# Optimization experiments

Hardware: AMD Instinct MI355X
Metric: run time of the kernel (lower is better)

## Reference

```python
import jax, jax.numpy as jnp
import numpy as np

D = 1024   # model dim (hard-coded in ClsNet)
H = 16     # num_heads
HD = D // H
FF = 2048  # torch TransformerEncoderLayer default dim_feedforward
B, LX, LY = 8, 512, 512
EPS = 1e-5
NEG = -1e9


def setup_inputs() -> dict:
    key = jax.random.key(0)
    ks = jax.random.split(key, 16)
    s = 0.02
    inp = {
        "x": jax.random.normal(ks[0], (B, LX, D), jnp.float32),
        "y": jax.random.normal(ks[1], (B, LY, D), jnp.float32),
        "cls": jax.random.normal(ks[2], (D,), jnp.float32) * s,
        "sep": jax.random.normal(ks[3], (D,), jnp.float32) * s,
        "px": jax.random.normal(ks[4], (D,), jnp.float32) * s,
        "py": jax.random.normal(ks[5], (D,), jnp.float32) * s,
        "Wqkv": jax.random.normal(ks[6], (3 * D, D), jnp.float32) * s,
        "bqkv": jnp.zeros((3 * D,), jnp.float32),
        "Wo": jax.random.normal(ks[7], (D, D), jnp.float32) * s,
        "bo": jnp.zeros((D,), jnp.float32),
        "W1": jax.random.normal(ks[8], (FF, D), jnp.float32) * s,
        "b1": jnp.zeros((FF,), jnp.float32),
        "W2": jax.random.normal(ks[9], (D, FF), jnp.float32) * s,
        "b2": jnp.zeros((D,), jnp.float32),
        "ln1_g": jnp.ones((D,), jnp.float32),
        "ln1_b": jnp.zeros((D,), jnp.float32),
        "ln2_g": jnp.ones((D,), jnp.float32),
        "ln2_b": jnp.zeros((D,), jnp.float32),
        "x_len": jax.random.randint(ks[10], (B,), 1, LX + 1, jnp.int32),
        "y_len": jax.random.randint(ks[11], (B,), 1, LY + 1, jnp.int32),
    }
    return inp


def _merge(x, y, cls, sep, px, py, x_len, y_len):
    # Vectorized version of ClsNet.merge: [CLS] x_i+px ... [SEP] y_i+py ... [SEP] pad...
    Bn, Lx, Dd = x.shape
    Ly = y.shape[1]
    S = Lx + Ly + 3
    pos = jnp.arange(S)[None, :]            # [1,S]
    lx = x_len[:, None]                     # [B,1]
    ly = y_len[:, None]
    is_cls = pos == 0                       # [1,S]
    is_x = (pos >= 1) & (pos <= lx)         # [B,S]
    is_sep1 = pos == lx + 1
    is_y = (pos >= lx + 2) & (pos <= lx + ly + 1)
    is_sep2 = pos == lx + ly + 2
    xi = jnp.clip(pos - 1, 0, Lx - 1)       # [1,S]
    yi = jnp.clip(pos - lx - 2, 0, Ly - 1)  # [B,S]
    xg = jnp.take_along_axis(x, xi[:, :, None], axis=1)  # [B,S,D] (broadcast batch)
    yg = jnp.take_along_axis(y, yi[:, :, None], axis=1)  # [B,S,D]
    seq = (jnp.where(is_x[..., None], xg + px, 0.0)
           + jnp.where(is_y[..., None], yg + py, 0.0)
           + is_cls[..., None] * cls
           + (is_sep1 | is_sep2)[..., None] * sep)       # [B,S,D]
    mask = is_cls | is_x | is_sep1 | is_y | is_sep2      # [B,S] True = valid token
    return seq, mask


def _ln(h, g, b):
    m = jnp.mean(h, axis=-1, keepdims=True)
    v = jnp.mean(jnp.square(h - m), axis=-1, keepdims=True)
    return (h - m) * jax.lax.rsqrt(v + EPS) * g + b


def _encoder_layer(seq, mask, Wqkv, bqkv, Wo, bo, W1, b1, W2, b2, ln1_g, ln1_b, ln2_g, ln2_b):
    Bn, S, Dd = seq.shape
    qkv = seq @ Wqkv.T + bqkv                              # [B,S,3D]
    q, k, v = jnp.split(qkv, 3, axis=-1)
    q = q.reshape(Bn, S, H, HD)
    k = k.reshape(Bn, S, H, HD)
    v = v.reshape(Bn, S, H, HD)
    bias = jnp.where(mask, 0.0, NEG)[:, None, None, :]     # padded KEYS masked out
    scores = jnp.einsum("bqhd,bkhd->bhqk", q, k) / np.sqrt(HD) + bias
    attn = jax.nn.softmax(scores, axis=-1)
    o = jnp.einsum("bhqk,bkhd->bqhd", attn, v).reshape(Bn, S, Dd)
    o = o @ Wo.T + bo
    h = _ln(seq + o, ln1_g, ln1_b)                          # post-norm (torch default)
    f = jax.nn.relu(h @ W1.T + b1) @ W2.T + b2
    return _ln(h + f, ln2_g, ln2_b)


def reference(x, y, cls, sep, px, py, Wqkv, bqkv, Wo, bo, W1, b1, W2, b2,
              ln1_g, ln1_b, ln2_g, ln2_b, x_len, y_len):
    seq, mask = _merge(x, y, cls, sep, px, py, x_len, y_len)
    out = _encoder_layer(seq, mask, Wqkv, bqkv, Wo, bo, W1, b1, W2, b2,
                         ln1_g, ln1_b, ln2_g, ln2_b)
    # torch code returns a[0] of the seq-first tensor -> the CLS position for all batches
    return out[:, 0, :]
```

## Files before the change

### kernel.cpp

```cpp
#include <hip/hip_runtime.h>
#include <hip/hip_bf16.h>

#define D_ 1024
#define H_ 16
#define FF_ 2048
#define B_ 8
#define S_ 1027
#define BS_ 8216
#define MPAD_ 8320
#define PSTR_ 1056
#define EPS_ 1e-5f
#define MAXGRID_ 512
#define NTILE_ 130
#define NBUCK_ 32

#define OFF_SEQ  0
#define OFF_RTHI 17039360
#define OFF_RTLO 17072128
#define OFF_S    17104896
#define OFF_P    17637376
#define OFF_CBAR 17907712
#define OFF_O0   20004864
#define OFF_ATT  20037632
#define OFF_F1   20070400
#define OFF_F2   20103168
#define OFF_BAR  20135936
#define OFF_Q0S  20140032
#define OFF_H0   20144128

typedef __hip_bfloat16 bf16;
typedef unsigned short u16;
typedef unsigned int u32;
typedef __attribute__((ext_vector_type(4))) float floatx4;
typedef __bf16 bf16x8 __attribute__((ext_vector_type(8)));

__device__ __forceinline__ float2 bfpair(u32 u) {
  union { u32 u; float f; } lo, hi;
  lo.u = u << 16; hi.u = u & 0xffff0000u;
  return make_float2(lo.f, hi.f);
}

__device__ __forceinline__ u32 f2bfbits(float f) {
  union { bf16 h; u16 u; } cv; cv.h = __float2bfloat16(f); return (u32)cv.u;
}

__device__ __forceinline__ void st_wt_f32(float* p, float v) {
  asm volatile("global_store_dword %0, %1, off sc0 sc1" :: "v"(p), "v"(v) : "memory");
}
__device__ __forceinline__ void st_wt_u16(u16* p, u32 v) {
  asm volatile("global_store_short %0, %1, off sc0 sc1" :: "v"(p), "v"(v) : "memory");
}
__device__ __forceinline__ void st_wt_v2(void* p, uint2 v) {
  asm volatile("global_store_dwordx2 %0, %1, off sc0 sc1" :: "v"(p), "v"(v) : "memory");
}
__device__ __forceinline__ void st_wt_f4(void* p, floatx4 v) {
  asm volatile("global_store_dwordx4 %0, %1, off sc0 sc1" :: "v"(p), "v"(v) : "memory");
}

__device__ __forceinline__ float blk_sum(float x, float* red) {
#pragma unroll
  for (int off = 32; off > 0; off >>= 1) x += __shfl_down(x, off, 64);
  __syncthreads();
  if ((threadIdx.x & 63) == 0) red[threadIdx.x >> 6] = x;
  __syncthreads();
  return red[0] + red[1] + red[2] + red[3];
}

__device__ __forceinline__ float blk_max(float x, float* red) {
#pragma unroll
  for (int off = 32; off > 0; off >>= 1) x = fmaxf(x, __shfl_down(x, off, 64));
  __syncthreads();
  if ((threadIdx.x & 63) == 0) red[threadIdx.x >> 6] = x;
  __syncthreads();
  return fmaxf(fmaxf(red[0], red[1]), fmaxf(red[2], red[3]));
}

__device__ __forceinline__ void gridbar(u32* bar, u32 phase) {
  asm volatile("s_waitcnt vmcnt(0) lgkmcnt(0)" ::: "memory");
  __syncthreads();
  if (threadIdx.x == 0) {
    __hip_atomic_fetch_add(bar + (blockIdx.x & (NBUCK_ - 1)) * 16, 1u,
                           __ATOMIC_RELAXED, __HIP_MEMORY_SCOPE_AGENT);
    u32* gen = bar + NBUCK_ * 16;
    if (blockIdx.x == 0) {
      const u32 target = (u32)gridDim.x * phase;
      int spins = 0;
      for (;;) {
        u32 s = 0;
#pragma unroll
        for (int i = 0; i < NBUCK_; ++i)
          s += __hip_atomic_load(bar + i * 16, __ATOMIC_RELAXED,
                                 __HIP_MEMORY_SCOPE_AGENT);
        if (s == target) break;
        __builtin_amdgcn_s_sleep(1);
        if (++spins > 300000) break;
      }
      __hip_atomic_store(gen, phase, __ATOMIC_RELAXED, __HIP_MEMORY_SCOPE_AGENT);
    } else {
      int spins = 0;
      while (__hip_atomic_load(gen, __ATOMIC_RELAXED,
                               __HIP_MEMORY_SCOPE_AGENT) < phase) {
        __builtin_amdgcn_s_sleep(2);
        if (++spins > 300000) break;
      }
    }
  }
  __syncthreads();
}

struct KP {
  const float *x, *y, *cls, *sep, *px, *py;
  const float *Wqkv, *bqkv, *Wo, *bo, *W1, *b1, *W2, *b2;
  const float *g1, *be1, *g2, *be2;
  const int *xl, *yl;
  bf16* seq; u16* RT_hi; u16* RT_lo; float* S; u16* P;
  float* cbar4; float* o0; float* att; bf16* f1; float* f2; float* out;
  u32* bar;
};

__global__ void __launch_bounds__(256, 2) mega_kernel(KP p) {
  __shared__ __align__(16) char smem_[33792];
  const int t = threadIdx.x;
  const int bid = blockIdx.x;
  const int G = gridDim.x;

  if (t == 0) __builtin_amdgcn_fence(__ATOMIC_ACQUIRE, "agent");
  gridbar(p.bar, 1);

  if (bid < 64) {
    const int h = bid >> 2, cc = bid & 3;
    float* cl = (float*)smem_;
    float* qs = (float*)(smem_ + 4096);
    *(float4*)&cl[t * 4] = ((const float4*)p.cls)[t];
    __syncthreads();
    const int r = t >> 2, j = t & 3;
    const float* wr = p.Wqkv + (size_t)(h * 64 + r) * D_;
    float acc = 0.f;
#pragma unroll 8
    for (int i = 0; i < 64; ++i) {
      float4 wv = *(const float4*)(wr + i * 16 + j * 4);
      const float* c4 = &cl[i * 16 + j * 4];
      acc += wv.x * c4[0] + wv.y * c4[1] + wv.z * c4[2] + wv.w * c4[3];
    }
    acc += __shfl_xor(acc, 1, 64);
    acc += __shfl_xor(acc, 2, 64);
    if (j == 0) qs[r] = (acc + p.bqkv[h * 64 + r]) * 0.125f;
    __syncthreads();
    const int c = cc * 256 + t;
    const float* Wk = p.Wqkv + (size_t)(D_ + h * 64) * D_ + c;
    float a2 = 0.f;
#pragma unroll 8
    for (int e = 0; e < 64; ++e) a2 += Wk[(size_t)e * D_] * qs[e];
    const u32 hb = f2bfbits(a2);
    union { u32 u; float f; } hv; hv.u = hb << 16;
    st_wt_u16(p.RT_hi + h * D_ + c, hb);
    st_wt_u16(p.RT_lo + h * D_ + c, f2bfbits(a2 - hv.f));
  } else {
    for (int m = bid - 64; m < BS_; m += G - 64) {
      const int b = m / S_;
      const int s = m - b * S_;
      const int lx = p.xl[b], ly = p.yl[b];
      const float* src = nullptr;
      const float* add = nullptr;
      if (s == 0) src = p.cls;
      else if (s <= lx) { src = p.x + ((size_t)b * 512 + (s - 1)) * D_; add = p.px; }
      else if (s == lx + 1) src = p.sep;
      else if (s <= lx + ly + 1) { src = p.y + ((size_t)b * 512 + (s - lx - 2)) * D_; add = p.py; }
      else if (s == lx + ly + 2) src = p.sep;
      if (!src) continue;
      float4 sv = ((const float4*)src)[t];
      if (add) {
        float4 av = ((const float4*)add)[t];
        sv.x += av.x; sv.y += av.y; sv.z += av.z; sv.w += av.w;
      }
      uint2 o;
      o.x = f2bfbits(sv.x) | (f2bfbits(sv.y) << 16);
      o.y = f2bfbits(sv.z) | (f2bfbits(sv.w) << 16);
      st_wt_v2((u16*)p.seq + (size_t)m * D_ + t * 4, o);
    }
  }
  gridbar(p.bar, 2);

  for (int wk = bid; wk < NTILE_; wk += G) {
    const int m0 = wk * 64;
    bool valid = false;
#pragma unroll
    for (int b = 0; b < B_; ++b) {
      int rs = b * S_, re = rs + p.xl[b] + p.yl[b] + 3;
      if (m0 < re && m0 + 64 > rs) valid = true;
    }
    if (!valid) continue;
    const int w = t >> 6, lane = t & 63, lane16 = lane & 15, quad = lane >> 4;
    const int row = m0 + w * 16 + lane16;
    const u16* arow = (const u16*)p.seq + (size_t)row * D_ + quad * 8;
    const u16* bh = p.RT_hi + lane16 * D_ + quad * 8;
    const u16* bl = p.RT_lo + lane16 * D_ + quad * 8;
    floatx4 acc = {};
#pragma unroll 4
    for (int kt = 0; kt < 32; ++kt) {
      bf16x8 a  = *(const bf16x8*)(arow + kt * 32);
      bf16x8 vh = *(const bf16x8*)(bh + kt * 32);
      bf16x8 vl = *(const bf16x8*)(bl + kt * 32);
      acc = __builtin_amdgcn_mfma_f32_16x16x32_bf16(a, vh, acc, 0, 0, 0);
      acc = __builtin_amdgcn_mfma_f32_16x16x32_bf16(a, vl, acc, 0, 0, 0);
    }
    st_wt_f4(&p.S[(size_t)lane16 * MPAD_ + m0 + w * 16 + quad * 4], acc);
  }
  gridbar(p.bar, 3);

  for (int wk = bid; wk < 128; wk += G) {
    const int h = wk >> 3, b = wk & 7;
    const int n = p.xl[b] + p.yl[b] + 3;
    float* sc = (float*)smem_;
    float* red = (float*)(smem_ + PSTR_ * 4);
    const float* Sp = p.S + (size_t)h * MPAD_ + b * S_;
    float lmax = -3.0e38f;
    for (int k = t; k < n; k += 256) {
      float s = Sp[k];
      sc[k] = s;
      lmax = fmaxf(lmax, s);
    }
    const float gmax = blk_max(lmax, red);
    float lsum = 0.f;
    for (int k = t; k < n; k += 256) {
      float pr = __expf(sc[k] - gmax);
      sc[k] = pr;
      lsum += pr;
    }
    const float inv = 1.0f / blk_sum(lsum, red);
    u16* Pp = p.P + (size_t)(h * 8 + b) * PSTR_;
    for (int k = t; k < PSTR_; k += 256)
      st_wt_u16(Pp + k, (k < n) ? f2bfbits(sc[k] * inv) : 0u);
    __syncthreads();
  }
  gridbar(p.bar, 4);

  for (int wk = bid; wk < 512; wk += G) {
    const int ct = wk & 15, b = (wk >> 4) & 7, piece = wk >> 7;
    const int c0 = ct * 64;
    const int n = p.xl[b] + p.yl[b] + 3;
    const int nkt = (n + 31) >> 5;
    const int KR0[4] = {0, 9, 17, 25};
    const int KR1[4] = {9, 17, 25, 33};
    const int kt0 = KR0[piece];
    const int kt1 = nkt < KR1[piece] ? nkt : KR1[piece];
    u16* tile = (u16*)smem_;
    const int w = t >> 6, lane = t & 63, lane16 = lane & 15, quad = lane >> 4;
    const int sk = t >> 3, scg = (t & 7) * 8;
    floatx4 acc = {};
    uint4 v = make_uint4(0u, 0u, 0u, 0u);
    if (kt0 < kt1 && kt0 * 32 + sk < n)
      v = *(const uint4*)((const u16*)p.seq + (size_t)((size_t)b * S_ + kt0 * 32 + sk) * D_ + c0 + scg);
    for (int kt = kt0; kt < kt1; ++kt) {
      u16* tb = tile + (kt & 1) * (32 * 68);
      *(uint2*)&tb[sk * 68 + scg]     = make_uint2(v.x, v.y);
      *(uint2*)&tb[sk * 68 + scg + 4] = make_uint2(v.z, v.w);
      v = make_uint4(0u, 0u, 0u, 0u);
      if (kt + 1 < kt1 && (kt + 1) * 32 + sk < n)
        v = *(const uint4*)((const u16*)p.seq + (size_t)((size_t)b * S_ + (kt + 1) * 32 + sk) * D_ + c0 + scg);
      __syncthreads();
      bf16x8 a = *(const bf16x8*)(p.P + (size_t)(lane16 * 8 + b) * PSTR_ + kt * 32 + quad * 8);
      union { bf16x8 v8; u16 u[8]; } bu;
#pragma unroll
      for (int j = 0; j < 8; ++j)
        bu.u[j] = tb[(quad * 8 + j) * 68 + w * 16 + lane16];
      acc = __builtin_amdgcn_mfma_f32_16x16x32_bf16(a, bu.v8, acc, 0, 0, 0);
    }
    float* dst = p.cbar4 + (size_t)piece * 131072;
#pragma unroll
    for (int r = 0; r < 4; ++r)
      st_wt_f32(&dst[(size_t)(b * 16 + quad * 4 + r) * D_ + c0 + w * 16 + lane16], acc[r]);
    __syncthreads();
  }
  gridbar(p.bar, 5);

  for (int wk = bid; wk < 256; wk += G) {
    float* lsf = (float*)smem_;
    const int hoff = ((wk * 4) >> 6) * D_;
#pragma unroll
    for (int i = 0; i < 8; ++i) {
      int flat = (t + i * 256) * 4;
      int b = flat >> 10, k = flat & 1023;
      size_t off = (size_t)b * 16384 + hoff + k;
      float4 a0 = *(const float4*)(p.cbar4 + off);
      float4 a1 = *(const float4*)(p.cbar4 + 131072 + off);
      float4 a2 = *(const float4*)(p.cbar4 + 262144 + off);
      float4 a3 = *(const float4*)(p.cbar4 + 393216 + off);
      a0.x += a1.x + a2.x + a3.x; a0.y += a1.y + a2.y + a3.y;
      a0.z += a1.z + a2.z + a3.z; a0.w += a1.w + a2.w + a3.w;
      *(float4*)&lsf[flat] = a0;
    }
    __syncthreads();
    const int w = t >> 6, l = t & 63;
    const int r = wk * 4 + w;
    const float* W = p.Wqkv + (size_t)2048 * 1024;
    float acc[8] = {};
#pragma unroll
    for (int ch = 0; ch < 4; ++ch) {
      float4 wv = *(const float4*)(W + (size_t)r * D_ + ch * 256 + l * 4);
#pragma unroll
      for (int b = 0; b < 8; ++b) {
        const float* pp = &lsf[b * D_ + ch * 256 + l * 4];
        acc[b] += wv.x * pp[0] + wv.y * pp[1] + wv.z * pp[2] + wv.w * pp[3];
      }
    }
#pragma unroll
    for (int off = 32; off > 0; off >>= 1)
#pragma unroll
      for (int b = 0; b < 8; ++b) acc[b] += __shfl_down(acc[b], off, 64);
    if (l == 0) {
      const float bs = p.bqkv[2048 + r];
#pragma unroll
      for (int b = 0; b < 8; ++b) st_wt_f32(&p.o0[(size_t)b * D_ + r], acc[b] + bs);
    }
    __syncthreads();
  }
  gridbar(p.bar, 6);

  for (int wk = bid; wk < 256; wk += G) {
    float* lsf = (float*)smem_;
#pragma unroll
    for (int i = 0; i < 8; ++i) {
      int flat = (t + i * 256) * 4;
      *(float4*)&lsf[flat] = *(const float4*)(p.o0 + flat);
    }
    __syncthreads();
    const int w = t >> 6, l = t & 63;
    const int r = wk * 4 + w;
    float acc[8] = {};
#pragma unroll
    for (int ch = 0; ch < 4; ++ch) {
      float4 wv = *(const float4*)(p.Wo + (size_t)r * D_ + ch * 256 + l * 4);
#pragma unroll
      for (int b = 0; b < 8; ++b) {
        const float* pp = &lsf[b * D_ + ch * 256 + l * 4];
        acc[b] += wv.x * pp[0] + wv.y * pp[1] + wv.z * pp[2] + wv.w * pp[3];
      }
    }
#pragma unroll
    for (int off = 32; off > 0; off >>= 1)
#pragma unroll
      for (int b = 0; b < 8; ++b) acc[b] += __shfl_down(acc[b], off, 64);
    if (l == 0) {
      const float bs = p.bo[r];
#pragma unroll
      for (int b = 0; b < 8; ++b) st_wt_f32(&p.att[(size_t)b * D_ + r], acc[b] + bs);
    }
    __syncthreads();
  }
  gridbar(p.bar, 7);

  for (int wk = bid; wk < 512; wk += G) {
    float* lsf = (float*)smem_;
#pragma unroll
    for (int i = 0; i < 8; ++i) {
      int flat = (t + i * 256) * 4;
      int b = flat >> 10, k = flat & 1023;
      float4 av = *(const float4*)(p.att + (size_t)b * D_ + k);
      float4 cv = *(const float4*)(p.cls + k);
      av.x += cv.x; av.y += cv.y; av.z += cv.z; av.w += cv.w;
      *(float4*)&lsf[flat] = av;
    }
    __syncthreads();
    const int w = t >> 6, l = t & 63;
#pragma unroll
    for (int bb = 2 * w; bb < 2 * w + 2; ++bb) {
      float s = 0.f;
#pragma unroll
      for (int kk = 0; kk < 16; ++kk) s += lsf[bb * 1024 + kk * 64 + l];
#pragma unroll
      for (int off = 32; off > 0; off >>= 1) s += __shfl_xor(s, off, 64);
      const float mean = s * (1.f / D_);
      float vv = 0.f;
#pragma unroll
      for (int kk = 0; kk < 16; ++kk) {
        float d = lsf[bb * 1024 + kk * 64 + l] - mean; vv += d * d;
      }
#pragma unroll
      for (int off = 32; off > 0; off >>= 1) vv += __shfl_xor(vv, off, 64);
      const float rs = rsqrtf(vv * (1.f / D_) + EPS_);
#pragma unroll
      for (int kk = 0; kk < 16; ++kk) {
        int idx = kk * 64 + l;
        lsf[bb * 1024 + idx] =
            (lsf[bb * 1024 + idx] - mean) * rs * p.g1[idx] + p.be1[idx];
      }
    }
    __syncthreads();
    const int r = wk * 4 + w;
    float acc[8] = {};
#pragma unroll
    for (int ch = 0; ch < 4; ++ch) {
      float4 wv = *(const float4*)(p.W1 + (size_t)r * D_ + ch * 256 + l * 4);
#pragma unroll
      for (int b = 0; b < 8; ++b) {
        const float* pp = &lsf[b * D_ + ch * 256 + l * 4];
        acc[b] += wv.x * pp[0] + wv.y * pp[1] + wv.z * pp[2] + wv.w * pp[3];
      }
    }
#pragma unroll
    for (int off = 32; off > 0; off >>= 1)
#pragma unroll
      for (int b = 0; b < 8; ++b) acc[b] += __shfl_down(acc[b], off, 64);
    if (l == 0) {
      const float bs = p.b1[r];
#pragma unroll
      for (int b = 0; b < 8; ++b)
        st_wt_u16((u16*)p.f1 + (size_t)b * FF_ + r, f2bfbits(fmaxf(acc[b] + bs, 0.f)));
    }
    __syncthreads();
  }
  gridbar(p.bar, 8);

  for (int wk = bid; wk < 256; wk += G) {
    u16* lsb = (u16*)smem_;
#pragma unroll
    for (int i = 0; i < 8; ++i) {
      int flat = (t + i * 256) * 8;
      *(uint4*)&lsb[flat] = *(const uint4*)((const u16*)p.f1 + flat);
    }
    __syncthreads();
    const int w = t >> 6, l = t & 63;
    const int r = wk * 4 + w;
    float acc[8] = {};
#pragma unroll
    for (int ch = 0; ch < 8; ++ch) {
      float4 wv = *(const float4*)(p.W2 + (size_t)r * FF_ + ch * 256 + l * 4);
#pragma unroll
      for (int b = 0; b < 8; ++b) {
        uint2 u = *(const uint2*)&lsb[b * FF_ + ch * 256 + l * 4];
        float2 p0 = bfpair(u.x), p1 = bfpair(u.y);
        acc[b] += wv.x * p0.x + wv.y * p0.y + wv.z * p1.x + wv.w * p1.y;
      }
    }
#pragma unroll
    for (int off = 32; off > 0; off >>= 1)
#pragma unroll
      for (int b = 0; b < 8; ++b) acc[b] += __shfl_down(acc[b], off, 64);
    if (l == 0) {
      const float bs = p.b2[r];
#pragma unroll
      for (int b = 0; b < 8; ++b) st_wt_f32(&p.f2[(size_t)b * D_ + r], acc[b] + bs);
    }
    __syncthreads();
  }
  gridbar(p.bar, 9);

  for (int wk = bid; wk < 8; wk += G) {
    float* v = (float*)smem_;
    float* red = (float*)(smem_ + D_ * 4);
    for (int i = t; i < D_; i += 256) v[i] = p.cls[i] + p.att[wk * D_ + i];
    __syncthreads();
    float ls = 0.f;
    for (int i = t; i < D_; i += 256) ls += v[i];
    const float mean1 = blk_sum(ls, red) * (1.f / D_);
    float lv = 0.f;
    for (int i = t; i < D_; i += 256) { float dk = v[i] - mean1; lv += dk * dk; }
    const float var1 = blk_sum(lv, red) * (1.f / D_);
    const float rs1 = rsqrtf(var1 + EPS_);
    for (int i = t; i < D_; i += 256) {
      float h0v = (v[i] - mean1) * rs1 * p.g1[i] + p.be1[i];
      v[i] = h0v + p.f2[wk * D_ + i];
    }
    __syncthreads();
    float ls2 = 0.f;
    for (int i = t; i < D_; i += 256) ls2 += v[i];
    const float mean2 = blk_sum(ls2, red) * (1.f / D_);
    float lv2 = 0.f;
    for (int i = t; i < D_; i += 256) { float dk = v[i] - mean2; lv2 += dk * dk; }
    const float var2 = blk_sum(lv2, red) * (1.f / D_);
    const float rs2 = rsqrtf(var2 + EPS_);
    for (int i = t; i < D_; i += 256)
      p.out[wk * D_ + i] = (v[i] - mean2) * rs2 * p.g2[i] + p.be2[i];
    __syncthreads();
  }
}

__device__ __forceinline__ float block_sum(float x, float* red) {
  const int t = threadIdx.x;
  __syncthreads();
  red[t] = x;
  __syncthreads();
  for (int s = 128; s > 0; s >>= 1) {
    if (t < s) red[t] += red[t + s];
    __syncthreads();
  }
  return red[0];
}

__device__ __forceinline__ float block_max(float x, float* red) {
  const int t = threadIdx.x;
  __syncthreads();
  red[t] = x;
  __syncthreads();
  for (int s = 128; s > 0; s >>= 1) {
    if (t < s) red[t] = fmaxf(red[t], red[t + s]);
    __syncthreads();
  }
  return red[0];
}

__global__ void __launch_bounds__(256) build_seq_kernel(
    const float* __restrict__ x, const float* __restrict__ y,
    const float* __restrict__ cls, const float* __restrict__ sep,
    const float* __restrict__ px, const float* __restrict__ py,
    const int* __restrict__ x_len, const int* __restrict__ y_len,
    bf16* __restrict__ seq) {
  const int m = blockIdx.x, t = threadIdx.x;
  const int b = m / S_;
  const int s = m - b * S_;
  if (b >= B_) return;
  const float* src = nullptr;
  const float* add = nullptr;
  const int lx = x_len[b], ly = y_len[b];
  if (s == 0) src = cls;
  else if (s <= lx) { src = x + ((size_t)b * 512 + (s - 1)) * D_; add = px; }
  else if (s == lx + 1) src = sep;
  else if (s <= lx + ly + 1) { src = y + ((size_t)b * 512 + (s - lx - 2)) * D_; add = py; }
  else if (s == lx + ly + 2) src = sep;
  if (!src) return;
  float4 sv = ((const float4*)src)[t];
  if (add) {
    float4 av = ((const float4*)add)[t];
    sv.x += av.x; sv.y += av.y; sv.z += av.z; sv.w += av.w;
  }
  uint2 o;
  o.x = f2bfbits(sv.x) | (f2bfbits(sv.y) << 16);
  o.y = f2bfbits(sv.z) | (f2bfbits(sv.w) << 16);
  ((uint2*)(seq + (size_t)m * D_))[t] = o;
}

__global__ void __launch_bounds__(256) qproj_kernel(
    const float* __restrict__ cls, const float* __restrict__ Wqkv,
    const float* __restrict__ bqkv, float* __restrict__ q0s) {
  __shared__ float cl[D_];
  const int t = threadIdx.x;
  *(float4*)&cl[t * 4] = ((const float4*)cls)[t];
  __syncthreads();
  const int w = t >> 6, l = t & 63;
  const int r = blockIdx.x * 4 + w;
  float acc = 0.f;
#pragma unroll
  for (int ch = 0; ch < 4; ++ch) {
    float4 wv = *(const float4*)(Wqkv + (size_t)r * D_ + ch * 256 + l * 4);
    const float* c4 = &cl[ch * 256 + l * 4];
    acc += wv.x * c4[0] + wv.y * c4[1] + wv.z * c4[2] + wv.w * c4[3];
  }
#pragma unroll
  for (int off = 32; off > 0; off >>= 1) acc += __shfl_down(acc, off, 64);
  if (l == 0) q0s[r] = (acc + bqkv[r]) * 0.125f;
}

__global__ void __launch_bounds__(256) rproj_kernel(
    const float* __restrict__ Wqkv, const float* __restrict__ q0s,
    u16* __restrict__ RT_hi, u16* __restrict__ RT_lo) {
  const int h = blockIdx.y, cc = blockIdx.x, t = threadIdx.x;
  __shared__ float qs[64];
  if (t < 64) qs[t] = q0s[h * 64 + t];
  __syncthreads();
  const int c = cc * 256 + t;
  const float* Wk = Wqkv + (size_t)(D_ + h * 64) * D_ + c;
  float acc = 0.f;
#pragma unroll 8
  for (int e = 0; e < 64; ++e) acc += Wk[(size_t)e * D_] * qs[e];
  const u32 hb = f2bfbits(acc);
  union { u32 u; float f; } hv; hv.u = hb << 16;
  RT_hi[h * D_ + c] = (u16)hb;
  RT_lo[h * D_ + c] = (u16)f2bfbits(acc - hv.f);
}

__global__ void __launch_bounds__(256) scores_kernel(
    const bf16* __restrict__ seq, const u16* __restrict__ RT_hi,
    const u16* __restrict__ RT_lo, const int* __restrict__ x_len,
    const int* __restrict__ y_len, float* __restrict__ S) {
  const int m0 = blockIdx.x * 64;
  bool valid = false;
#pragma unroll
  for (int b = 0; b < B_; ++b) {
    int rs = b * S_, re = rs + x_len[b] + y_len[b] + 3;
    if (m0 < re && m0 + 64 > rs) valid = true;
  }
  if (!valid) return;
  const int t = threadIdx.x;
  const int w = t >> 6, lane = t & 63, lane16 = lane & 15, quad = lane >> 4;
  const int row = m0 + w * 16 + lane16;
  const u16* arow = (const u16*)seq + (size_t)row * D_ + quad * 8;
  const u16* bh = RT_hi + lane16 * D_ + quad * 8;
  const u16* bl = RT_lo + lane16 * D_ + quad * 8;
  floatx4 acc = {};
#pragma unroll 4
  for (int kt = 0; kt < 32; ++kt) {
    bf16x8 a  = *(const bf16x8*)(arow + kt * 32);
    bf16x8 vh = *(const bf16x8*)(bh + kt * 32);
    bf16x8 vl = *(const bf16x8*)(bl + kt * 32);
    acc = __builtin_amdgcn_mfma_f32_16x16x32_bf16(a, vh, acc, 0, 0, 0);
    acc = __builtin_amdgcn_mfma_f32_16x16x32_bf16(a, vl, acc, 0, 0, 0);
  }
  *(floatx4*)&S[(size_t)lane16 * MPAD_ + m0 + w * 16 + quad * 4] = acc;
}

__global__ void __launch_bounds__(256) softmax_kernel(
    const float* __restrict__ S, const int* __restrict__ x_len,
    const int* __restrict__ y_len, u16* __restrict__ P) {
  const int h = blockIdx.x, b = blockIdx.y, t = threadIdx.x;
  const int n = x_len[b] + y_len[b] + 3;
  __shared__ float sc[PSTR_];
  __shared__ float red[256];
  const float* Sp = S + (size_t)h * MPAD_ + b * S_;
  float lmax = -3.0e38f;
  for (int k = t; k < n; k += 256) {
    float s = Sp[k];
    sc[k] = s;
    lmax = fmaxf(lmax, s);
  }
  const float gmax = block_max(lmax, red);
  float lsum = 0.f;
  for (int k = t; k < n; k += 256) {
    float p = __expf(sc[k] - gmax);
    sc[k] = p;
    lsum += p;
  }
  const float inv = 1.0f / block_sum(lsum, red);
  u16* Pp = P + (size_t)(h * 8 + b) * PSTR_;
  for (int k = t; k < PSTR_; k += 256)
    Pp[k] = (k < n) ? (u16)f2bfbits(sc[k] * inv) : (u16)0;
}

__global__ void __launch_bounds__(256) cbar_kernel(
    const bf16* __restrict__ seq, const u16* __restrict__ P,
    const int* __restrict__ x_len, const int* __restrict__ y_len,
    float* __restrict__ cbar) {
  const int ct = blockIdx.x, b = blockIdx.y, t = threadIdx.x;
  const int c0 = ct * 64;
  const int n = x_len[b] + y_len[b] + 3;
  const int nkt = (n + 31) >> 5;
  __shared__ u16 tile[32 * 68];
  const int w = t >> 6, lane = t & 63, lane16 = lane & 15, quad = lane >> 4;
  const int sk = t >> 3, scg = (t & 7) * 8;
  floatx4 acc = {};
  for (int kt = 0; kt < nkt; ++kt) {
    const int k0 = kt * 32;
    __syncthreads();
    uint4 v = make_uint4(0u, 0u, 0u, 0u);
    if (k0 + sk < n)
      v = *(const uint4*)((const u16*)seq + (size_t)(b * S_ + k0 + sk) * D_ + c0 + scg);
    *(uint2*)&tile[sk * 68 + scg]     = make_uint2(v.x, v.y);
    *(uint2*)&tile[sk * 68 + scg + 4] = make_uint2(v.z, v.w);
    __syncthreads();
    bf16x8 a = *(const bf16x8*)(P + (size_t)(lane16 * 8 + b) * PSTR_ + k0 + quad * 8);
    union { bf16x8 v; u16 u[8]; } bu;
#pragma unroll
    for (int j = 0; j < 8; ++j)
      bu.u[j] = tile[(quad * 8 + j) * 68 + w * 16 + lane16];
    acc = __builtin_amdgcn_mfma_f32_16x16x32_bf16(a, bu.v, acc, 0, 0, 0);
  }
#pragma unroll
  for (int r = 0; r < 4; ++r)
    cbar[(size_t)(b * 16 + quad * 4 + r) * D_ + c0 + w * 16 + lane16] = acc[r];
}

template <int K, int N, int BSTR, bool INBF, bool OUTBF, bool RELU, bool PERHEAD>
__global__ void __launch_bounds__(256) gemv8_kernel(
    const void* __restrict__ in_, const float* __restrict__ W,
    const float* __restrict__ bias, void* __restrict__ out_) {
  const int t = threadIdx.x;
  const int hoff = PERHEAD ? ((blockIdx.x * 4) >> 6) * D_ : 0;
  __shared__ u16 lsb[INBF ? 8 * K : 1];
  __shared__ float lsf[INBF ? 1 : 8 * K];
  if (INBF) {
    const u16* in = (const u16*)in_;
    const int per = 8 * K / (256 * 8);
#pragma unroll
    for (int i = 0; i < per; ++i) {
      int flat = (t + i * 256) * 8;
      int b = flat / K, k = flat % K;
      *(uint4*)&lsb[flat] = *(const uint4*)(in + (size_t)b * BSTR + hoff + k);
    }
  } else {
    const float* in = (const float*)in_;
    const int per = 8 * K / (256 * 4);
#pragma unroll
    for (int i = 0; i < per; ++i) {
      int flat = (t + i * 256) * 4;
      int b = flat / K, k = flat % K;
      *(float4*)&lsf[flat] = *(const float4*)(in + (size_t)b * BSTR + hoff + k);
    }
  }
  __syncthreads();
  const int w = t >> 6, l = t & 63;
  const int r = blockIdx.x * 4 + w;
  float acc[8] = {};
#pragma unroll
  for (int ch = 0; ch < K / 256; ++ch) {
    float4 wv = *(const float4*)(W + (size_t)r * K + ch * 256 + l * 4);
#pragma unroll
    for (int b = 0; b < 8; ++b) {
      float i0, i1, i2, i3;
      if (INBF) {
        uint2 u = *(const uint2*)&lsb[b * K + ch * 256 + l * 4];
        float2 p0 = bfpair(u.x), p1 = bfpair(u.y);
        i0 = p0.x; i1 = p0.y; i2 = p1.x; i3 = p1.y;
      } else {
        const float* p = &lsf[b * K + ch * 256 + l * 4];
        i0 = p[0]; i1 = p[1]; i2 = p[2]; i3 = p[3];
      }
      acc[b] += wv.x * i0 + wv.y * i1 + wv.z * i2 + wv.w * i3;
    }
  }
#pragma unroll
  for (int off = 32; off > 0; off >>= 1)
#pragma unroll
    for (int b = 0; b < 8; ++b) acc[b] += __shfl_down(acc[b], off, 64);
  if (l == 0) {
    const float bs = bias[r];
#pragma unroll
    for (int b = 0; b < 8; ++b) {
      float v = acc[b] + bs;
      if (RELU) v = fmaxf(v, 0.f);
      if (OUTBF) ((bf16*)out_)[(size_t)b * N + r] = __float2bfloat16(v);
      else       ((float*)out_)[(size_t)b * N + r] = v;
    }
  }
}

template <bool SECOND>
__global__ void __launch_bounds__(256) ln_kernel(
    const float* __restrict__ cls, const float* __restrict__ a,
    const float* __restrict__ bvec, const float* __restrict__ g,
    const float* __restrict__ be, float* __restrict__ out) {
  const int b = blockIdx.x, t = threadIdx.x;
  __shared__ float v[D_];
  __shared__ float red[256];
  for (int i = t; i < D_; i += 256) {
    float val;
    if (SECOND) val = a[b * D_ + i] + bvec[b * D_ + i];
    else        val = cls[i] + a[b * D_ + i];
    v[i] = val;
  }
  __syncthreads();
  float ls = 0.f;
  for (int i = t; i < D_; i += 256) ls += v[i];
  const float mean = block_sum(ls, red) * (1.f / D_);
  float lv = 0.f;
  for (int i = t; i < D_; i += 256) { float dk = v[i] - mean; lv += dk * dk; }
  const float var = block_sum(lv, red) * (1.f / D_);
  const float rs = rsqrtf(var + EPS_);
  for (int i = t; i < D_; i += 256)
    out[b * D_ + i] = (v[i] - mean) * rs * g[i] + be[i];
}

extern "C" void kernel_launch(void* const* d_in, const int* in_sizes, int n_in,
                              void* d_out, int out_size, void* d_ws, size_t ws_size,
                              hipStream_t stream) {
  (void)in_sizes; (void)n_in; (void)out_size; (void)ws_size;
  const float* x    = (const float*)d_in[0];
  const float* y    = (const float*)d_in[1];
  const float* cls  = (const float*)d_in[2];
  const float* sep  = (const float*)d_in[3];
  const float* px   = (const float*)d_in[4];
  const float* py   = (const float*)d_in[5];
  const float* Wqkv = (const float*)d_in[6];
  const float* bqkv = (const float*)d_in[7];
  const float* Wo   = (const float*)d_in[8];
  const float* bo   = (const float*)d_in[9];
  const float* W1   = (const float*)d_in[10];
  const float* b1   = (const float*)d_in[11];
  const float* W2   = (const float*)d_in[12];
  const float* b2   = (const float*)d_in[13];
  const float* g1   = (const float*)d_in[14];
  const float* be1  = (const float*)d_in[15];
  const float* g2   = (const float*)d_in[16];
  const float* be2  = (const float*)d_in[17];
  const int* xl     = (const int*)d_in[18];
  const int* yl     = (const int*)d_in[19];

  char* ws = (char*)d_ws;
  bf16*  seq   = (bf16*)(ws + OFF_SEQ);
  u16*   RT_hi = (u16*)(ws + OFF_RTHI);
  u16*   RT_lo = (u16*)(ws + OFF_RTLO);
  float* S     = (float*)(ws + OFF_S);
  u16*   P     = (u16*)(ws + OFF_P);
  float* cbar4 = (float*)(ws + OFF_CBAR);
  float* o0    = (float*)(ws + OFF_O0);
  float* att   = (float*)(ws + OFF_ATT);
  bf16*  f1    = (bf16*)(ws + OFF_F1);
  float* f2    = (float*)(ws + OFF_F2);
  u32*   bar   = (u32*)(ws + OFF_BAR);
  float* q0s   = (float*)(ws + OFF_Q0S);
  float* h0    = (float*)(ws + OFF_H0);

  KP kp;
  kp.x = x; kp.y = y; kp.cls = cls; kp.sep = sep; kp.px = px; kp.py = py;
  kp.Wqkv = Wqkv; kp.bqkv = bqkv; kp.Wo = Wo; kp.bo = bo;
  kp.W1 = W1; kp.b1 = b1; kp.W2 = W2; kp.b2 = b2;
  kp.g1 = g1; kp.be1 = be1; kp.g2 = g2; kp.be2 = be2;
  kp.xl = xl; kp.yl = yl;
  kp.seq = seq; kp.RT_hi = RT_hi; kp.RT_lo = RT_lo;
  kp.S = S; kp.P = P; kp.cbar4 = cbar4;
  kp.o0 = o0; kp.att = att; kp.f1 = f1; kp.f2 = f2;
  kp.out = (float*)d_out;
  kp.bar = bar;

  static int mega_grid = -2;
  if (mega_grid == -2) {
    int nb = 0, ncu = 256;
    hipDeviceProp_t props;
    if (hipGetDeviceProperties(&props, 0) == hipSuccess)
      ncu = props.multiProcessorCount;
    if (hipOccupancyMaxActiveBlocksPerMultiprocessor(&nb, mega_kernel, 256, 0) ==
            hipSuccess && nb > 0) {
      long g = (long)nb * ncu;
      mega_grid = (int)(g < MAXGRID_ ? g : MAXGRID_);
    } else {
      mega_grid = -1;
    }
    if (mega_grid < 72) mega_grid = -1;
  }

  if (mega_grid > 0) {
    hipMemsetAsync(ws + OFF_BAR, 0, 4096, stream);
    mega_kernel<<<mega_grid, 256, 0, stream>>>(kp);
  } else {
    build_seq_kernel<<<MPAD_, 256, 0, stream>>>(x, y, cls, sep, px, py, xl, yl, seq);
    qproj_kernel<<<256, 256, 0, stream>>>(cls, Wqkv, bqkv, q0s);
    rproj_kernel<<<dim3(4, 16), 256, 0, stream>>>(Wqkv, q0s, RT_hi, RT_lo);
    scores_kernel<<<130, 256, 0, stream>>>(seq, RT_hi, RT_lo, xl, yl, S);
    softmax_kernel<<<dim3(16, 8), 256, 0, stream>>>(S, xl, yl, P);
    cbar_kernel<<<dim3(16, 8), 256, 0, stream>>>(seq, P, xl, yl, cbar4);
    gemv8_kernel<1024, 1024, 16384, false, false, false, true>
        <<<256, 256, 0, stream>>>(cbar4, Wqkv + (size_t)2048 * 1024, bqkv + 2048, o0);
    gemv8_kernel<1024, 1024, 1024, false, false, false, false>
        <<<256, 256, 0, stream>>>(o0, Wo, bo, att);
    ln_kernel<false><<<B_, 256, 0, stream>>>(cls, att, nullptr, g1, be1, h0);
    gemv8_kernel<1024, 2048, 1024, false, true, true, false>
        <<<512, 256, 0, stream>>>(h0, W1, b1, f1);
    gemv8_kernel<2048, 1024, 2048, true, false, false, false>
        <<<256, 256, 0, stream>>>(f1, W2, b2, f2);
    ln_kernel<true><<<B_, 256, 0, stream>>>(nullptr, h0, f2, g2, be2, (float*)d_out);
  }
}
```

Before: 211.2 us.

## Trim grid barriers, flatten barrier polling, and accumulate cbar with atomics

Drops the initial grid barrier and replaces the generation-flag barrier with one where every block polls 8 bucket counters directly. The cbar stage now accumulates into a single buffer with float atomicAdd, after zeroing it during the softmax phase. This removes the 4-piece partial buffers, their reduction in the next stage and one grid barrier. The sequence-build loop also processes two rows per iteration, issuing loads before stores. The trade-offs are more atomic traffic and more contention from all blocks polling the counters, and the summation order now varies between runs.

Measured after the change: 224.7 us. 6.4% more time.

```diff
diff --git a/kernel.cpp b/kernel.cpp
--- a/kernel.cpp
+++ b/kernel.cpp
@@ -12,7 +12,6 @@
 #define EPS_ 1e-5f
 #define MAXGRID_ 512
 #define NTILE_ 130
-#define NBUCK_ 32
 
 #define OFF_SEQ  0
 #define OFF_RTHI 17039360
@@ -79,30 +78,19 @@
   asm volatile("s_waitcnt vmcnt(0) lgkmcnt(0)" ::: "memory");
   __syncthreads();
   if (threadIdx.x == 0) {
-    __hip_atomic_fetch_add(bar + (blockIdx.x & (NBUCK_ - 1)) * 16, 1u,
+    __hip_atomic_fetch_add(bar + (blockIdx.x & 7) * 16, 1u,
                            __ATOMIC_RELAXED, __HIP_MEMORY_SCOPE_AGENT);
-    u32* gen = bar + NBUCK_ * 16;
-    if (blockIdx.x == 0) {
-      const u32 target = (u32)gridDim.x * phase;
-      int spins = 0;
-      for (;;) {
-        u32 s = 0;
-#pragma unroll
-        for (int i = 0; i < NBUCK_; ++i)
-          s += __hip_atomic_load(bar + i * 16, __ATOMIC_RELAXED,
-                                 __HIP_MEMORY_SCOPE_AGENT);
-        if (s == target) break;
-        __builtin_amdgcn_s_sleep(1);
-        if (++spins > 300000) break;
-      }
-      __hip_atomic_store(gen, phase, __ATOMIC_RELAXED, __HIP_MEMORY_SCOPE_AGENT);
-    } else {
-      int spins = 0;
-      while (__hip_atomic_load(gen, __ATOMIC_RELAXED,
-                               __HIP_MEMORY_SCOPE_AGENT) < phase) {
-        __builtin_amdgcn_s_sleep(2);
-        if (++spins > 300000) break;
-      }
+    const u32 target = (u32)gridDim.x * phase;
+    int spins = 0;
+    for (;;) {
+      u32 s = 0;
+#pragma unroll
+      for (int i = 0; i < 8; ++i)
+        s += __hip_atomic_load(bar + i * 16, __ATOMIC_RELAXED,
+                               __HIP_MEMORY_SCOPE_AGENT);
+      if (s >= target) break;
+      __builtin_amdgcn_s_sleep(2);
+      if (++spins > 400000) break;
     }
   }
   __syncthreads();
@@ -114,9 +102,24 @@
   const float *g1, *be1, *g2, *be2;
   const int *xl, *yl;
   bf16* seq; u16* RT_hi; u16* RT_lo; float* S; u16* P;
-  float* cbar4; float* o0; float* att; bf16* f1; float* f2; float* out;
+  float* cbar; float* o0; float* att; bf16* f1; float* f2; float* out;
   u32* bar;
 };
+
+__device__ __forceinline__ const float* row_src(const KP& p, int m,
+                                                const int* lx8, const int* ly8,
+                                                const float** add) {
+  const int b = m / S_;
+  const int s = m - b * S_;
+  const int lx = lx8[b], ly = ly8[b];
+  *add = nullptr;
+  if (s == 0) return p.cls;
+  if (s <= lx) { *add = p.px; return p.x + ((size_t)b * 512 + (s - 1)) * D_; }
+  if (s == lx + 1) return p.sep;
+  if (s <= lx + ly + 1) { *add = p.py; return p.y + ((size_t)b * 512 + (s - lx - 2)) * D_; }
+  if (s == lx + ly + 2) return p.sep;
+  return nullptr;
+}
 
 __global__ void __launch_bounds__(256, 2) mega_kernel(KP p) {
   __shared__ __align__(16) char smem_[33792];
@@ -125,7 +128,7 @@
   const int G = gridDim.x;
 
   if (t == 0) __builtin_amdgcn_fence(__ATOMIC_ACQUIRE, "agent");
-  gridbar(p.bar, 1);
+  __syncthreads();
 
   if (bid < 64) {
     const int h = bid >> 2, cc = bid & 3;
@@ -156,30 +159,37 @@
     st_wt_u16(p.RT_hi + h * D_ + c, hb);
     st_wt_u16(p.RT_lo + h * D_ + c, f2bfbits(a2 - hv.f));
   } else {
-    for (int m = bid - 64; m < BS_; m += G - 64) {
-      const int b = m / S_;
-      const int s = m - b * S_;
-      const int lx = p.xl[b], ly = p.yl[b];
-      const float* src = nullptr;
-      const float* add = nullptr;
-      if (s == 0) src = p.cls;
-      else if (s <= lx) { src = p.x + ((size_t)b * 512 + (s - 1)) * D_; add = p.px; }
-      else if (s == lx + 1) src = p.sep;
-      else if (s <= lx + ly + 1) { src = p.y + ((size_t)b * 512 + (s - lx - 2)) * D_; add = p.py; }
-      else if (s == lx + ly + 2) src = p.sep;
-      if (!src) continue;
-      float4 sv = ((const float4*)src)[t];
-      if (add) {
-        float4 av = ((const float4*)add)[t];
-        sv.x += av.x; sv.y += av.y; sv.z += av.z; sv.w += av.w;
+    int lx8[8], ly8[8];
+#pragma unroll
+    for (int b = 0; b < 8; ++b) { lx8[b] = p.xl[b]; ly8[b] = p.yl[b]; }
+    const int stride = G - 64;
+    for (int m0 = bid - 64; m0 < BS_; m0 += 2 * stride) {
+      const int m1 = m0 + stride;
+      const float *ad0, *ad1 = nullptr;
+      const float* s0 = row_src(p, m0, lx8, ly8, &ad0);
+      const float* s1 = (m1 < BS_) ? row_src(p, m1, lx8, ly8, &ad1) : nullptr;
+      float4 v0, a0v, v1, a1v;
+      if (s0) v0 = ((const float4*)s0)[t];
+      if (ad0) a0v = ((const float4*)ad0)[t];
+      if (s1) v1 = ((const float4*)s1)[t];
+      if (ad1) a1v = ((const float4*)ad1)[t];
+      if (s0) {
+        if (ad0) { v0.x += a0v.x; v0.y += a0v.y; v0.z += a0v.z; v0.w += a0v.w; }
+        uint2 o;
+        o.x = f2bfbits(v0.x) | (f2bfbits(v0.y) << 16);
+        o.y = f2bfbits(v0.z) | (f2bfbits(v0.w) << 16);
+        st_wt_v2((u16*)p.seq + (size_t)m0 * D_ + t * 4, o);
       }
-      uint2 o;
-      o.x = f2bfbits(sv.x) | (f2bfbits(sv.y) << 16);
-      o.y = f2bfbits(sv.z) | (f2bfbits(sv.w) << 16);
-      st_wt_v2((u16*)p.seq + (size_t)m * D_ + t * 4, o);
-    }
-  }
-  gridbar(p.bar, 2);
+      if (s1) {
+        if (ad1) { v1.x += a1v.x; v1.y += a1v.y; v1.z += a1v.z; v1.w += a1v.w; }
+        uint2 o;
+        o.x = f2bfbits(v1.x) | (f2bfbits(v1.y) << 16);
+        o.y = f2bfbits(v1.z) | (f2bfbits(v1.w) << 16);
+        st_wt_v2((u16*)p.seq + (size_t)m1 * D_ + t * 4, o);
+      }
+    }
+  }
+  gridbar(p.bar, 1);
 
   for (int wk = bid; wk < NTILE_; wk += G) {
     const int m0 = wk * 64;
@@ -206,8 +216,13 @@
     }
     st_wt_f4(&p.S[(size_t)lane16 * MPAD_ + m0 + w * 16 + quad * 4], acc);
   }
-  gridbar(p.bar, 3);
-
+  gridbar(p.bar, 2);
+
+  {
+    floatx4 z = {};
+    for (int idx = bid * 256 + t; idx < 32768; idx += G * 256)
+      st_wt_f4(p.cbar + (size_t)idx * 4, z);
+  }
   for (int wk = bid; wk < 128; wk += G) {
     const int h = wk >> 3, b = wk & 7;
     const int n = p.xl[b] + p.yl[b] + 3;
@@ -233,7 +248,7 @@
       st_wt_u16(Pp + k, (k < n) ? f2bfbits(sc[k] * inv) : 0u);
     __syncthreads();
   }
-  gridbar(p.bar, 4);
+  gridbar(p.bar, 3);
 
   for (int wk = bid; wk < 512; wk += G) {
     const int ct = wk & 15, b = (wk >> 4) & 7, piece = wk >> 7;
@@ -251,6 +266,7 @@
     uint4 v = make_uint4(0u, 0u, 0u, 0u);
     if (kt0 < kt1 && kt0 * 32 + sk < n)
       v = *(const uint4*)((const u16*)p.seq + (size_t)((size_t)b * S_ + kt0 * 32 + sk) * D_ + c0 + scg);
+    bool any = (kt0 < kt1);
     for (int kt = kt0; kt < kt1; ++kt) {
       u16* tb = tile + (kt & 1) * (32 * 68);
       *(uint2*)&tb[sk * 68 + scg]     = make_uint2(v.x, v.y);
@@ -266,13 +282,14 @@
         bu.u[j] = tb[(quad * 8 + j) * 68 + w * 16 + lane16];
       acc = __builtin_amdgcn_mfma_f32_16x16x32_bf16(a, bu.v8, acc, 0, 0, 0);
     }
-    float* dst = p.cbar4 + (size_t)piece * 131072;
-#pragma unroll
-    for (int r = 0; r < 4; ++r)
-      st_wt_f32(&dst[(size_t)(b * 16 + quad * 4 + r) * D_ + c0 + w * 16 + lane16], acc[r]);
-    __syncthreads();
-  }
-  gridbar(p.bar, 5);
+    if (any) {
+#pragma unroll
+      for (int r = 0; r < 4; ++r)
+        atomicAdd(&p.cbar[(size_t)(b * 16 + quad * 4 + r) * D_ + c0 + w * 16 + lane16], acc[r]);
+    }
+    __syncthreads();
+  }
+  gridbar(p.bar, 4);
 
   for (int wk = bid; wk < 256; wk += G) {
     float* lsf = (float*)smem_;
@@ -281,14 +298,7 @@
     for (int i = 0; i < 8; ++i) {
       int flat = (t + i * 256) * 4;
       int b = flat >> 10, k = flat & 1023;
-      size_t off = (size_t)b * 16384 + hoff + k;
-      float4 a0 = *(const float4*)(p.cbar4 + off);
-      float4 a1 = *(const float4*)(p.cbar4 + 131072 + off);
-      float4 a2 = *(const float4*)(p.cbar4 + 262144 + off);
-      float4 a3 = *(const float4*)(p.cbar4 + 393216 + off);
-      a0.x += a1.x + a2.x + a3.x; a0.y += a1.y + a2.y + a3.y;
-      a0.z += a1.z + a2.z + a3.z; a0.w += a1.w + a2.w + a3.w;
-      *(float4*)&lsf[flat] = a0;
+      *(float4*)&lsf[flat] = *(const float4*)(p.cbar + (size_t)b * 16384 + hoff + k);
     }
     __syncthreads();
     const int w = t >> 6, l = t & 63;
@@ -315,7 +325,7 @@
     }
     __syncthreads();
   }
-  gridbar(p.bar, 6);
+  gridbar(p.bar, 5);
 
   for (int wk = bid; wk < 256; wk += G) {
     float* lsf = (float*)smem_;
@@ -348,7 +358,7 @@
     }
     __syncthreads();
   }
-  gridbar(p.bar, 7);
+  gridbar(p.bar, 6);
 
   for (int wk = bid; wk < 512; wk += G) {
     float* lsf = (float*)smem_;
@@ -410,7 +420,7 @@
     }
     __syncthreads();
   }
-  gridbar(p.bar, 8);
+  gridbar(p.bar, 7);
 
   for (int wk = bid; wk < 256; wk += G) {
     u16* lsb = (u16*)smem_;
@@ -444,7 +454,7 @@
     }
     __syncthreads();
   }
-  gridbar(p.bar, 9);
+  gridbar(p.bar, 8);
 
   for (int wk = bid; wk < 8; wk += G) {
     float* v = (float*)smem_;
@@ -780,7 +790,7 @@
   u16*   RT_lo = (u16*)(ws + OFF_RTLO);
   float* S     = (float*)(ws + OFF_S);
   u16*   P     = (u16*)(ws + OFF_P);
-  float* cbar4 = (float*)(ws + OFF_CBAR);
+  float* cbar  = (float*)(ws + OFF_CBAR);
   float* o0    = (float*)(ws + OFF_O0);
   float* att   = (float*)(ws + OFF_ATT);
   bf16*  f1    = (bf16*)(ws + OFF_F1);
@@ -796,7 +806,7 @@
   kp.g1 = g1; kp.be1 = be1; kp.g2 = g2; kp.be2 = be2;
   kp.xl = xl; kp.yl = yl;
   kp.seq = seq; kp.RT_hi = RT_hi; kp.RT_lo = RT_lo;
-  kp.S = S; kp.P = P; kp.cbar4 = cbar4;
+  kp.S = S; kp.P = P; kp.cbar = cbar;
   kp.o0 = o0; kp.att = att; kp.f1 = f1; kp.f2 = f2;
   kp.out = (float*)d_out;
   kp.bar = bar;
@@ -826,9 +836,9 @@
     rproj_kernel<<<dim3(4, 16), 256, 0, stream>>>(Wqkv, q0s, RT_hi, RT_lo);
     scores_kernel<<<130, 256, 0, stream>>>(seq, RT_hi, RT_lo, xl, yl, S);
     softmax_kernel<<<dim3(16, 8), 256, 0, stream>>>(S, xl, yl, P);
-    cbar_kernel<<<dim3(16, 8), 256, 0, stream>>>(seq, P, xl, yl, cbar4);
+    cbar_kernel<<<dim3(16, 8), 256, 0, stream>>>(seq, P, xl, yl, cbar);
     gemv8_kernel<1024, 1024, 16384, false, false, false, true>
-        <<<256, 256, 0, stream>>>(cbar4, Wqkv + (size_t)2048 * 1024, bqkv + 2048, o0);
+        <<<256, 256, 0, stream>>>(cbar, Wqkv + (size_t)2048 * 1024, bqkv + 2048, o0);
     gemv8_kernel<1024, 1024, 1024, false, false, false, false>
         <<<256, 256, 0, stream>>>(o0, Wo, bo, att);
     ln_kernel<false><<<B_, 256, 0, stream>>>(cls, att, nullptr, g1, be1, h0);
```
